# Kernel tuning notes

Measured on AMD Instinct MI355X. Metric: run time of the kernel, lower is better.

Reference implementation:

```python
import jax, jax.numpy as jnp
import numpy as np

D_MODEL = 1024
D_OUT = 128  # output_embed_size (head dim)

def setup_inputs() -> dict:
    key = jax.random.key(0)
    ks = jax.random.split(key, 4)
    x = jax.random.normal(ks[0], (2, 4096, D_MODEL), dtype=jnp.float32)
    # weights mimic nn.init.normal_(std=0.02), biases zero
    qW_w = 0.02 * jax.random.normal(ks[1], (D_OUT, D_MODEL), dtype=jnp.float32)
    kW_w = 0.02 * jax.random.normal(ks[2], (D_OUT, D_MODEL), dtype=jnp.float32)
    vW_w = 0.02 * jax.random.normal(ks[3], (D_OUT, D_MODEL), dtype=jnp.float32)
    zb = jnp.zeros((D_OUT,), dtype=jnp.float32)
    return {"x": x, "qW_w": qW_w, "qW_b": zb, "kW_w": kW_w, "kW_b": zb,
            "vW_w": vW_w, "vW_b": zb}

def reference(x, qW_w, qW_b, kW_w, kW_b, vW_w, vW_b):
    # Linear: y = x @ W^T + b
    Q = jnp.einsum('bsd,ed->bse', x, qW_w) + qW_b  # [B,S,E]
    K = jnp.einsum('bsd,ed->bse', x, kW_w) + kW_b
    V = jnp.einsum('bsd,ed->bse', x, vW_w) + vW_b
    scale = 1.0 / jnp.sqrt(jnp.float32(D_OUT))
    attention = jnp.einsum('bqe,bke->bqk', Q, K) * scale  # [B,S,S], NO softmax
    output = jnp.einsum('bqk,bke->bqe', attention, V)     # [B,S,E]
    return output
```

## Files before the change

### kernel.cpp

```cpp
#include <hip/hip_runtime.h>

#define SS 4096
#define DD 1024
#define EE 128
#define SCALE 0.08838834764831845f

typedef __bf16 bf16x8 __attribute__((ext_vector_type(8)));
typedef float  f32x4  __attribute__((ext_vector_type(4)));

__device__ __forceinline__ void gload16(const void* g, void* l) {
  __builtin_amdgcn_global_load_lds(
      (const __attribute__((address_space(1))) void*)g,
      (__attribute__((address_space(3))) void*)l, 16, 0, 0);
}

__global__ __launch_bounds__(256) void wcast_kernel(
    const float* __restrict__ qW, const float* __restrict__ kW,
    const float* __restrict__ vW, __bf16* __restrict__ Wb)
{
  const int m = blockIdx.y;
  const float* src = (m == 0) ? qW : (m == 1 ? kW : vW);
  const size_t o = ((size_t)blockIdx.x * 256 + threadIdx.x) * 8;
  float4 u0 = *(const float4*)&src[o];
  float4 u1 = *(const float4*)&src[o + 4];
  bf16x8 v = { (__bf16)u0.x, (__bf16)u0.y, (__bf16)u0.z, (__bf16)u0.w,
               (__bf16)u1.x, (__bf16)u1.y, (__bf16)u1.z, (__bf16)u1.w };
  *(bf16x8*)&Wb[(size_t)m * EE * DD + o] = v;
}

__global__ __launch_bounds__(256, 3) void proj_kernel(
    const float* __restrict__ x, const __bf16* __restrict__ Wb,
    const float* __restrict__ qB, const float* __restrict__ kB,
    const float* __restrict__ vB,
    __bf16* __restrict__ Qbf, __bf16* __restrict__ KT, __bf16* __restrict__ VT)
{
  __shared__ __attribute__((aligned(16))) __bf16 ldsA[2][64 * 64];
  __shared__ __attribute__((aligned(16))) __bf16 ldsB[2][64 * 64];

  const int tid  = threadIdx.x;
  const int w    = tid >> 6, lane = tid & 63;
  const int l15  = lane & 15, l4 = lane >> 4;
  const int wr   = w >> 1, wc = w & 1;

  const int id   = blockIdx.x;
  const int swz  = (id & 7) * 96 + (id >> 3);
  const int rt   = swz / 6, ct = swz % 6;
  const int row0 = rt * 64;
  const int g0   = ct * 64;

  const int arow = tid >> 2;
  const int aseg = tid & 3;
  const int ars  = arow & 7;
  const float* gA = x + (size_t)(row0 + arow) * DD + aseg * 16;

  const int bRow = lane >> 3;
  const int cB   = (lane & 7) ^ bRow;
  const __bf16* gB = Wb + (size_t)(g0 + w * 16 + bRow) * DD + cB * 8;

  f32x4 acc[2][2] = {};
  f32x4 rA0[4], rA1[4];

#define AISSUE(RS, T) {                                                      \
    const float* g_ = gA + (T) * 64;                                         \
    RS[0] = *(const f32x4*)(g_);      RS[1] = *(const f32x4*)(g_ + 4);       \
    RS[2] = *(const f32x4*)(g_ + 8);  RS[3] = *(const f32x4*)(g_ + 12); }

#define AWRITE(P, RS) {                                                      \
    bf16x8 v0_ = { (__bf16)RS[0][0], (__bf16)RS[0][1], (__bf16)RS[0][2],     \
                   (__bf16)RS[0][3], (__bf16)RS[1][0], (__bf16)RS[1][1],     \
                   (__bf16)RS[1][2], (__bf16)RS[1][3] };                     \
    bf16x8 v1_ = { (__bf16)RS[2][0], (__bf16)RS[2][1], (__bf16)RS[2][2],     \
                   (__bf16)RS[2][3], (__bf16)RS[3][0], (__bf16)RS[3][1],     \
                   (__bf16)RS[3][2], (__bf16)RS[3][3] };                     \
    *(bf16x8*)&ldsA[P][arow * 64 + (((aseg * 2)     ^ ars) << 3)] = v0_;     \
    *(bf16x8*)&ldsA[P][arow * 64 + (((aseg * 2 + 1) ^ ars) << 3)] = v1_; }

#define BSTAGE(P, T) {                                                       \
    gload16(gB + (T) * 64,                   &ldsB[P][(w * 16    ) * 64]);   \
    gload16(gB + (T) * 64 + (size_t)8 * DD,  &ldsB[P][(w * 16 + 8) * 64]); }

#define COMPUTE(P) {                                                         \
    const int rs7 = l15 & 7;                                                 \
    _Pragma("unroll") for (int ks = 0; ks < 2; ++ks) {                       \
      const int so = ((ks * 4 + l4) ^ rs7) << 3;                             \
      bf16x8 a0 = *(const bf16x8*)&ldsA[P][(wr * 32      + l15) * 64 + so];  \
      bf16x8 a1 = *(const bf16x8*)&ldsA[P][(wr * 32 + 16 + l15) * 64 + so];  \
      bf16x8 b0 = *(const bf16x8*)&ldsB[P][(wc * 32      + l15) * 64 + so];  \
      bf16x8 b1 = *(const bf16x8*)&ldsB[P][(wc * 32 + 16 + l15) * 64 + so];  \
      acc[0][0] = __builtin_amdgcn_mfma_f32_16x16x32_bf16(a0,b0,acc[0][0],0,0,0); \
      acc[0][1] = __builtin_amdgcn_mfma_f32_16x16x32_bf16(a0,b1,acc[0][1],0,0,0); \
      acc[1][0] = __builtin_amdgcn_mfma_f32_16x16x32_bf16(a1,b0,acc[1][0],0,0,0); \
      acc[1][1] = __builtin_amdgcn_mfma_f32_16x16x32_bf16(a1,b1,acc[1][1],0,0,0); \
    } }

#define HEADBAR(VN) {                                                        \
    asm volatile("s_waitcnt vmcnt(" #VN ") lgkmcnt(0)" ::: "memory");        \
    __builtin_amdgcn_s_barrier();                                            \
    asm volatile("" ::: "memory"); }

  AISSUE(rA0, 0);
  BSTAGE(0, 0);
  __builtin_amdgcn_sched_barrier(0);
  AISSUE(rA1, 1);
  __builtin_amdgcn_sched_barrier(0);
  AWRITE(0, rA0);

  for (int t = 0; t < 14; t += 2) {
    HEADBAR(4);
    COMPUTE(0);
    BSTAGE(1, t + 1);
    __builtin_amdgcn_sched_barrier(0);
    AISSUE(rA0, t + 2);
    __builtin_amdgcn_sched_barrier(0);
    AWRITE(1, rA1);
    HEADBAR(4);
    COMPUTE(1);
    BSTAGE(0, t + 2);
    __builtin_amdgcn_sched_barrier(0);
    AISSUE(rA1, t + 3);
    __builtin_amdgcn_sched_barrier(0);
    AWRITE(0, rA0);
  }
  HEADBAR(4);
  COMPUTE(0);
  BSTAGE(1, 15);
  __builtin_amdgcn_sched_barrier(0);
  AWRITE(1, rA1);
  HEADBAR(0);
  COMPUTE(1);
#undef AISSUE
#undef AWRITE
#undef BSTAGE
#undef COMPUTE
#undef HEADBAR
  __syncthreads();

  const float* bias = (g0 < 128) ? qB : (g0 < 256 ? kB : vB);
  const int bofs = (g0 < 128) ? g0 : (g0 < 256 ? g0 - 128 : g0 - 256);

  if (ct < 2) {
    #pragma unroll
    for (int m = 0; m < 2; ++m)
      #pragma unroll
      for (int n = 0; n < 2; ++n) {
        const int col = wc * 32 + n * 16 + l15;
        const float bv = bias[bofs + col];
        #pragma unroll
        for (int r = 0; r < 4; ++r) {
          const int row = row0 + wr * 32 + m * 16 + l4 * 4 + r;
          Qbf[(size_t)row * EE + g0 + col] = (__bf16)(acc[m][n][r] + bv);
        }
      }
  } else {
    __bf16* Tb = (__bf16*)ldsA;
    #pragma unroll
    for (int m = 0; m < 2; ++m)
      #pragma unroll
      for (int n = 0; n < 2; ++n) {
        const int tc = wc * 32 + n * 16 + l15;
        const float bv = bias[bofs + tc];
        #pragma unroll
        for (int r = 0; r < 4; ++r) {
          const int rl = wr * 32 + m * 16 + l4 * 4 + r;
          Tb[tc * 64 + (((rl >> 3) ^ (tc & 7)) << 3) + (rl & 7)] =
              (__bf16)(acc[m][n][r] + bv);
        }
      }
    __syncthreads();
    const int col = tid >> 2, p2 = tid & 3;
    const int b = row0 >> 12, s0 = row0 & 4095;
    __bf16* dst = (ct < 4)
        ? &KT[((size_t)b * EE + (ct - 2) * 64 + col) * SS + s0]
        : &VT[((size_t)b * EE + (ct - 4) * 64 + col) * SS + s0];
    #pragma unroll
    for (int j = 0; j < 2; ++j) {
      const int ch = p2 * 2 + j;
      bf16x8 v = *(const bf16x8*)&Tb[col * 64 + ((ch ^ (col & 7)) << 3)];
      *(bf16x8*)&dst[ch * 8] = v;
    }
  }
}

__global__ __launch_bounds__(256) void ktv_kernel(
    const __bf16* __restrict__ KT, const __bf16* __restrict__ VT,
    float* __restrict__ part)
{
  const int c = blockIdx.x, fh = blockIdx.y, b = blockIdx.z;
  const int tid = threadIdx.x;
  const int w = tid >> 6, lane = tid & 63;
  const int l15 = lane & 15, l4 = lane >> 4;
  const int s0 = c * 64;
  const int fbase = fh * 64 + w * 16;
  const __bf16* Kb = KT + (size_t)b * EE * SS;
  const __bf16* Vb = VT + (size_t)b * EE * SS;

  f32x4 acc[8] = {};
  #pragma unroll
  for (int ks = 0; ks < 2; ++ks) {
    const int s = s0 + ks * 32 + 8 * l4;
    bf16x8 bv = *(const bf16x8*)&Vb[(size_t)(fbase + l15) * SS + s];
    #pragma unroll
    for (int i = 0; i < 8; ++i) {
      bf16x8 av = *(const bf16x8*)&Kb[(size_t)(i * 16 + l15) * SS + s];
      acc[i] = __builtin_amdgcn_mfma_f32_16x16x32_bf16(av, bv, acc[i], 0, 0, 0);
    }
  }
  float* P = part + (size_t)(b * 64 + c) * 16384;
  #pragma unroll
  for (int i = 0; i < 8; ++i)
    #pragma unroll
    for (int r = 0; r < 4; ++r) {
      int e = i * 16 + l4 * 4 + r;
      int f = fbase + l15;
      P[e * 128 + f] = acc[i][r];
    }
}

__global__ __launch_bounds__(256) void reduce_kernel(
    const float* __restrict__ part, __bf16* __restrict__ MT)
{
  const int b = blockIdx.y;
  const int e = blockIdx.x * 2 + (threadIdx.x >> 7);
  const int f = threadIdx.x & 127;
  float s = 0.f;
  for (int cc = 0; cc < 64; ++cc)
    s += part[(size_t)(b * 64 + cc) * 16384 + e * 128 + f];
  MT[((size_t)b * EE + f) * EE + e] = (__bf16)(SCALE * s);
}

__global__ __launch_bounds__(128) void qm_kernel(
    const __bf16* __restrict__ Qbf, const __bf16* __restrict__ MT,
    float* __restrict__ out)
{
  const int b = blockIdx.y;
  const int tid = threadIdx.x;
  const int w = tid >> 6, lane = tid & 63;
  const int l15 = lane & 15, l4 = lane >> 4;
  const int row0 = blockIdx.x * 32 + w * 16;
  const __bf16* Qb = Qbf + (size_t)b * SS * EE;
  const __bf16* Mb = MT + (size_t)b * EE * EE;

  f32x4 acc[8] = {};
  #pragma unroll
  for (int ks = 0; ks < 4; ++ks) {
    const int e = ks * 32 + 8 * l4;
    bf16x8 av = *(const bf16x8*)&Qb[(size_t)(row0 + l15) * EE + e];
    #pragma unroll
    for (int j = 0; j < 8; ++j) {
      bf16x8 bv = *(const bf16x8*)&Mb[(size_t)(j * 16 + l15) * EE + e];
      acc[j] = __builtin_amdgcn_mfma_f32_16x16x32_bf16(av, bv, acc[j], 0, 0, 0);
    }
  }
  #pragma unroll
  for (int j = 0; j < 8; ++j)
    #pragma unroll
    for (int r = 0; r < 4; ++r) {
      int srow = row0 + l4 * 4 + r;
      int f = j * 16 + l15;
      out[((size_t)b * SS + srow) * EE + f] = acc[j][r];
    }
}

extern "C" void kernel_launch(void* const* d_in, const int* in_sizes, int n_in,
                              void* d_out, int out_size, void* d_ws, size_t ws_size,
                              hipStream_t stream) {
  const float* x  = (const float*)d_in[0];
  const float* qW = (const float*)d_in[1];
  const float* qB = (const float*)d_in[2];
  const float* kW = (const float*)d_in[3];
  const float* kB = (const float*)d_in[4];
  const float* vW = (const float*)d_in[5];
  const float* vB = (const float*)d_in[6];
  float* out = (float*)d_out;

  char* base = (char*)d_ws;
  __bf16* Wb  = (__bf16*)(base);
  __bf16* Qbf = (__bf16*)(base + (1u  << 20));
  __bf16* KT  = (__bf16*)(base + (3u  << 20));
  __bf16* VT  = (__bf16*)(base + (5u  << 20));
  float*  part= (float*) (base + (7u  << 20));
  __bf16* MT  = (__bf16*)(base + (15u << 20));

  wcast_kernel <<<dim3(64, 3),    256, 0, stream>>>(qW, kW, vW, Wb);
  proj_kernel  <<<dim3(768),      256, 0, stream>>>(x, Wb, qB, kB, vB, Qbf, KT, VT);
  ktv_kernel   <<<dim3(64, 2, 2), 256, 0, stream>>>(KT, VT, part);
  reduce_kernel<<<dim3(64, 2),    256, 0, stream>>>(part, MT);
  qm_kernel    <<<dim3(128, 2),   128, 0, stream>>>(Qbf, MT, out);
}
```

Baseline: 41.72 us.

## Use two-wave proj blocks with 64x32 per-wave tiles and fold scale into Q

The projection kernel moves from 256 threads (4 waves in a 2x2 layout of 32x32 tiles) to 128 threads, where each wave computes a 64x32 tile. Each wave now reads A fragments once per k-step and reuses them across more MFMAs. The loads of x are rearranged into eight row-strided float4 reads, staged into LDS as bf16x4 writes, and B staging issues four loads per wave. The attention scale moves from the reduce kernel into the Q projection epilogue. The change targets LDS read traffic per MFMA but halves the number of waves per block, which may reduce latency hiding, and the higher register use may lower occupancy.

```diff
diff --git a/kernel.cpp b/kernel.cpp
--- a/kernel.cpp
+++ b/kernel.cpp
@@ -6,6 +6,7 @@
 #define SCALE 0.08838834764831845f
 
 typedef __bf16 bf16x8 __attribute__((ext_vector_type(8)));
+typedef __bf16 bf16x4 __attribute__((ext_vector_type(4)));
 typedef float  f32x4  __attribute__((ext_vector_type(4)));
 
 __device__ __forceinline__ void gload16(const void* g, void* l) {
@@ -28,7 +29,7 @@
   *(bf16x8*)&Wb[(size_t)m * EE * DD + o] = v;
 }
 
-__global__ __launch_bounds__(256, 3) void proj_kernel(
+__global__ __launch_bounds__(128, 2) void proj_kernel(
     const float* __restrict__ x, const __bf16* __restrict__ Wb,
     const float* __restrict__ qB, const float* __restrict__ kB,
     const float* __restrict__ vB,
@@ -40,7 +41,6 @@
   const int tid  = threadIdx.x;
   const int w    = tid >> 6, lane = tid & 63;
   const int l15  = lane & 15, l4 = lane >> 4;
-  const int wr   = w >> 1, wc = w & 1;
 
   const int id   = blockIdx.x;
   const int swz  = (id & 7) * 96 + (id >> 3);
@@ -48,49 +48,50 @@
   const int row0 = rt * 64;
   const int g0   = ct * 64;
 
-  const int arow = tid >> 2;
-  const int aseg = tid & 3;
-  const int ars  = arow & 7;
-  const float* gA = x + (size_t)(row0 + arow) * DD + aseg * 16;
+  const int arow0 = w * 4 + (lane >> 4);
+  const int acolv = lane & 15;
+  const float* gA = x + (size_t)(row0 + arow0) * DD + acolv * 4;
+  const int acc16 = acolv >> 1, ahalf = acolv & 1;
 
   const int bRow = lane >> 3;
   const int cB   = (lane & 7) ^ bRow;
-  const __bf16* gB = Wb + (size_t)(g0 + w * 16 + bRow) * DD + cB * 8;
-
-  f32x4 acc[2][2] = {};
-  f32x4 rA0[4], rA1[4];
+  const __bf16* gB = Wb + (size_t)(g0 + w * 32 + bRow) * DD + cB * 8;
+
+  f32x4 acc[4][2] = {};
+  f32x4 rA0[8], rA1[8];
 
 #define AISSUE(RS, T) {                                                      \
     const float* g_ = gA + (T) * 64;                                         \
-    RS[0] = *(const f32x4*)(g_);      RS[1] = *(const f32x4*)(g_ + 4);       \
-    RS[2] = *(const f32x4*)(g_ + 8);  RS[3] = *(const f32x4*)(g_ + 12); }
+    _Pragma("unroll") for (int j = 0; j < 8; ++j)                            \
+      RS[j] = *(const f32x4*)(g_ + (size_t)j * 8 * DD);                      }
 
 #define AWRITE(P, RS) {                                                      \
-    bf16x8 v0_ = { (__bf16)RS[0][0], (__bf16)RS[0][1], (__bf16)RS[0][2],     \
-                   (__bf16)RS[0][3], (__bf16)RS[1][0], (__bf16)RS[1][1],     \
-                   (__bf16)RS[1][2], (__bf16)RS[1][3] };                     \
-    bf16x8 v1_ = { (__bf16)RS[2][0], (__bf16)RS[2][1], (__bf16)RS[2][2],     \
-                   (__bf16)RS[2][3], (__bf16)RS[3][0], (__bf16)RS[3][1],     \
-                   (__bf16)RS[3][2], (__bf16)RS[3][3] };                     \
-    *(bf16x8*)&ldsA[P][arow * 64 + (((aseg * 2)     ^ ars) << 3)] = v0_;     \
-    *(bf16x8*)&ldsA[P][arow * 64 + (((aseg * 2 + 1) ^ ars) << 3)] = v1_; }
+    _Pragma("unroll") for (int j = 0; j < 8; ++j) {                          \
+      bf16x4 v_ = { (__bf16)RS[j][0], (__bf16)RS[j][1],                      \
+                    (__bf16)RS[j][2], (__bf16)RS[j][3] };                    \
+      const int r_ = arow0 + j * 8;                                          \
+      *(bf16x4*)&ldsA[P][r_ * 64 + (((acc16 ^ (r_ & 7)) << 3) + ahalf * 4)]  \
+          = v_;                                                              \
+    } }
 
 #define BSTAGE(P, T) {                                                       \
-    gload16(gB + (T) * 64,                   &ldsB[P][(w * 16    ) * 64]);   \
-    gload16(gB + (T) * 64 + (size_t)8 * DD,  &ldsB[P][(w * 16 + 8) * 64]); }
+    _Pragma("unroll") for (int j = 0; j < 4; ++j)                            \
+      gload16(gB + (T) * 64 + (size_t)j * 8 * DD,                            \
+              &ldsB[P][(w * 32 + j * 8) * 64]);                              }
 
 #define COMPUTE(P) {                                                         \
     const int rs7 = l15 & 7;                                                 \
     _Pragma("unroll") for (int ks = 0; ks < 2; ++ks) {                       \
       const int so = ((ks * 4 + l4) ^ rs7) << 3;                             \
-      bf16x8 a0 = *(const bf16x8*)&ldsA[P][(wr * 32      + l15) * 64 + so];  \
-      bf16x8 a1 = *(const bf16x8*)&ldsA[P][(wr * 32 + 16 + l15) * 64 + so];  \
-      bf16x8 b0 = *(const bf16x8*)&ldsB[P][(wc * 32      + l15) * 64 + so];  \
-      bf16x8 b1 = *(const bf16x8*)&ldsB[P][(wc * 32 + 16 + l15) * 64 + so];  \
-      acc[0][0] = __builtin_amdgcn_mfma_f32_16x16x32_bf16(a0,b0,acc[0][0],0,0,0); \
-      acc[0][1] = __builtin_amdgcn_mfma_f32_16x16x32_bf16(a0,b1,acc[0][1],0,0,0); \
-      acc[1][0] = __builtin_amdgcn_mfma_f32_16x16x32_bf16(a1,b0,acc[1][0],0,0,0); \
-      acc[1][1] = __builtin_amdgcn_mfma_f32_16x16x32_bf16(a1,b1,acc[1][1],0,0,0); \
+      bf16x8 af[4], bq[2];                                                   \
+      _Pragma("unroll") for (int m = 0; m < 4; ++m)                          \
+        af[m] = *(const bf16x8*)&ldsA[P][(m * 16 + l15) * 64 + so];          \
+      _Pragma("unroll") for (int n = 0; n < 2; ++n)                          \
+        bq[n] = *(const bf16x8*)&ldsB[P][(w * 32 + n * 16 + l15) * 64 + so]; \
+      _Pragma("unroll") for (int m = 0; m < 4; ++m)                          \
+        _Pragma("unroll") for (int n = 0; n < 2; ++n)                        \
+          acc[m][n] = __builtin_amdgcn_mfma_f32_16x16x32_bf16(               \
+              af[m], bq[n], acc[m][n], 0, 0, 0);                             \
     } }
 
 #define HEADBAR(VN) {                                                        \
@@ -106,14 +107,14 @@
   AWRITE(0, rA0);
 
   for (int t = 0; t < 14; t += 2) {
-    HEADBAR(4);
+    HEADBAR(8);
     COMPUTE(0);
     BSTAGE(1, t + 1);
     __builtin_amdgcn_sched_barrier(0);
     AISSUE(rA0, t + 2);
     __builtin_amdgcn_sched_barrier(0);
     AWRITE(1, rA1);
-    HEADBAR(4);
+    HEADBAR(8);
     COMPUTE(1);
     BSTAGE(0, t + 2);
     __builtin_amdgcn_sched_barrier(0);
@@ -121,7 +122,7 @@
     __builtin_amdgcn_sched_barrier(0);
     AWRITE(0, rA0);
   }
-  HEADBAR(4);
+  HEADBAR(8);
   COMPUTE(0);
   BSTAGE(1, 15);
   __builtin_amdgcn_sched_barrier(0);
@@ -140,41 +141,42 @@
 
   if (ct < 2) {
     #pragma unroll
-    for (int m = 0; m < 2; ++m)
+    for (int m = 0; m < 4; ++m)
       #pragma unroll
       for (int n = 0; n < 2; ++n) {
-        const int col = wc * 32 + n * 16 + l15;
+        const int col = w * 32 + n * 16 + l15;
         const float bv = bias[bofs + col];
         #pragma unroll
         for (int r = 0; r < 4; ++r) {
-          const int row = row0 + wr * 32 + m * 16 + l4 * 4 + r;
-          Qbf[(size_t)row * EE + g0 + col] = (__bf16)(acc[m][n][r] + bv);
+          const int row = row0 + m * 16 + l4 * 4 + r;
+          Qbf[(size_t)row * EE + g0 + col] =
+              (__bf16)((acc[m][n][r] + bv) * SCALE);
         }
       }
   } else {
     __bf16* Tb = (__bf16*)ldsA;
     #pragma unroll
-    for (int m = 0; m < 2; ++m)
+    for (int m = 0; m < 4; ++m)
       #pragma unroll
       for (int n = 0; n < 2; ++n) {
-        const int tc = wc * 32 + n * 16 + l15;
+        const int tc = w * 32 + n * 16 + l15;
         const float bv = bias[bofs + tc];
         #pragma unroll
         for (int r = 0; r < 4; ++r) {
-          const int rl = wr * 32 + m * 16 + l4 * 4 + r;
+          const int rl = m * 16 + l4 * 4 + r;
           Tb[tc * 64 + (((rl >> 3) ^ (tc & 7)) << 3) + (rl & 7)] =
               (__bf16)(acc[m][n][r] + bv);
         }
       }
     __syncthreads();
-    const int col = tid >> 2, p2 = tid & 3;
+    const int col = tid >> 1, p2 = tid & 1;
     const int b = row0 >> 12, s0 = row0 & 4095;
     __bf16* dst = (ct < 4)
         ? &KT[((size_t)b * EE + (ct - 2) * 64 + col) * SS + s0]
         : &VT[((size_t)b * EE + (ct - 4) * 64 + col) * SS + s0];
     #pragma unroll
-    for (int j = 0; j < 2; ++j) {
-      const int ch = p2 * 2 + j;
+    for (int j = 0; j < 4; ++j) {
+      const int ch = p2 * 4 + j;
       bf16x8 v = *(const bf16x8*)&Tb[col * 64 + ((ch ^ (col & 7)) << 3)];
       *(bf16x8*)&dst[ch * 8] = v;
     }
@@ -225,7 +227,7 @@
   float s = 0.f;
   for (int cc = 0; cc < 64; ++cc)
     s += part[(size_t)(b * 64 + cc) * 16384 + e * 128 + f];
-  MT[((size_t)b * EE + f) * EE + e] = (__bf16)(SCALE * s);
+  MT[((size_t)b * EE + f) * EE + e] = (__bf16)s;
 }
 
 __global__ __launch_bounds__(128) void qm_kernel(
@@ -282,7 +284,7 @@
   __bf16* MT  = (__bf16*)(base + (15u << 20));
 
   wcast_kernel <<<dim3(64, 3),    256, 0, stream>>>(qW, kW, vW, Wb);
-  proj_kernel  <<<dim3(768),      256, 0, stream>>>(x, Wb, qB, kB, vB, Qbf, KT, VT);
+  proj_kernel  <<<dim3(768),      128, 0, stream>>>(x, Wb, qB, kB, vB, Qbf, KT, VT);
   ktv_kernel   <<<dim3(64, 2, 2), 256, 0, stream>>>(KT, VT, part);
   reduce_kernel<<<dim3(64, 2),    256, 0, stream>>>(part, MT);
   qm_kernel    <<<dim3(128, 2),   128, 0, stream>>>(Qbf, MT, out);
```

Result: no change. 41.14 us (median of 2 runs) (-1.4%).
